# Performance work log

Hardware: AMD Instinct MI355X
Metric: run time of the kernel (lower is better)

Reference implementation:

```python
import jax, jax.numpy as jnp
import numpy as np

TOP_K = 2

def setup_inputs() -> dict:
    key = jax.random.key(0)
    k1, k2 = jax.random.split(key)
    T, D, E = 16384, 2048, 64  # num_tokens, d_model, num_experts
    x = jax.random.normal(k1, (T, D), dtype=jnp.float32)
    Wg = jax.random.normal(k2, (D, E), dtype=jnp.float32) / np.sqrt(D)
    return {"x": x, "Wg": Wg}

def reference(x, Wg):
    T, E = x.shape[0], Wg.shape[1]
    # gate logits + softmax over experts
    logits = x @ Wg                                   # [T, E]
    probs = jax.nn.softmax(logits, axis=-1)           # [T, E]
    # top-k expert selection, renormalize selected weights
    top_vals, top_idx = jax.lax.top_k(probs, TOP_K)   # [T, K]
    top_vals = top_vals / jnp.sum(top_vals, axis=-1, keepdims=True)
    # scatter sparse gate weights into dense [T, E]
    rows = jnp.arange(T)[:, None]                     # [T, 1]
    gate_weights = jnp.zeros_like(probs).at[rows, top_idx].set(top_vals)
    # load-balance aux loss: E * sum_e f_e * P_e
    mask = jnp.sum(jax.nn.one_hot(top_idx, E, dtype=probs.dtype), axis=1)  # [T, E]
    f = jnp.mean(mask, axis=0)    # fraction of tokens routed to each expert
    P = jnp.mean(probs, axis=0)   # mean router prob per expert
    aux_loss = E * jnp.sum(f * P)
    return gate_weights, top_idx, aux_loss
```

## Files before the change

kernel.cpp:

```cpp
#include <hip/hip_runtime.h>


typedef __attribute__((ext_vector_type(8))) _Float16 half8;
typedef __attribute__((ext_vector_type(4))) float f32x4;

constexpr int DD  = 2048;
constexpr int EE  = 64;
constexpr int BM  = 16;
constexpr int BK  = 128;
constexpr int NCH = DD / BK;

#define WVM(N) asm volatile("s_waitcnt vmcnt(" #N ")" ::: "memory")
#define BAR()  asm volatile("s_barrier" ::: "memory")

__global__ __launch_bounds__(256) void wsplit_kernel(
    const float* __restrict__ Wg, _Float16* __restrict__ wF)
{
    __shared__ float xl[32][65];
    const int tid = threadIdx.x;
    const int kc  = blockIdx.x;
    const int k0  = kc * 32;
#pragma unroll
    for (int r = 0; r < 2; ++r) {
        int slot = tid + r * 256;
        int row = slot >> 4, c4 = (slot & 15) << 2;
        *(float4*)&xl[row][c4] = *(const float4*)&Wg[(size_t)(k0 + row) * EE + c4];
    }
    __syncthreads();
    const int t = tid >> 6, l = tid & 63;
    const int e  = t * 16 + (l & 15);
    const int kl = (l >> 4) * 8;
    half8 hh, ll;
#pragma unroll
    for (int j = 0; j < 8; ++j) {
        float v = xl[kl + j][e];
        _Float16 h = (_Float16)v;
        hh[j] = h;
        ll[j] = (_Float16)((v - (float)h) * 4096.f);
    }
    const size_t base = (size_t)(kc * 8 + t * 2) * 512 + (size_t)l * 8;
    *(half8*)&wF[base]       = hh;
    *(half8*)&wF[base + 512] = ll;
}

__global__ __launch_bounds__(256, 4) void gate_kernel(
    const float* __restrict__ x, const _Float16* __restrict__ wF,
    float* __restrict__ gate_out, float* __restrict__ idx_out,
    float* __restrict__ pSum, float* __restrict__ pCnt)
{
    __shared__ __align__(16) union {
        float xs[3][BM][BK];
        struct { float red[4][BM][68]; float auxsm[2][4][64]; } ep;
    } sm;

    const int tid  = threadIdx.x;
    const int kq   = tid >> 6;
    const int lane = tid & 63;
    const size_t tok0 = (size_t)blockIdx.x * BM;
    const float* xg = x + tok0 * DD;

    auto stageX = [&](int buf, int c) {
#pragma unroll
        for (int r = 0; r < 2; ++r) {
            int slot = tid + r * 256;
            int row  = slot >> 5;
            int cb   = (slot & 31) << 4;
            int sb   = cb ^ ((row & 7) << 5);
            __builtin_amdgcn_global_load_lds(
                xg + (size_t)row * DD + c * BK + (sb >> 2),
                &sm.xs[buf][row][cb >> 2], 16, 0, 0);
        }
    };

    f32x4 aH[4], aL[4];
#pragma unroll
    for (int t = 0; t < 4; ++t) {
        aH[t] = (f32x4){0.f, 0.f, 0.f, 0.f};
        aL[t] = (f32x4){0.f, 0.f, 0.f, 0.f};
    }

    const int rrow = lane & 15;
    const int rb   = (kq * 128 + ((lane >> 4) * 32)) ^ ((rrow & 7) << 5);

    auto compute = [&](int buf, int c) {
        const _Float16* wb = wF + (size_t)(c * 4 + kq) * 4096 + (size_t)lane * 8;
        half8 wh[4], wl[4];
#pragma unroll
        for (int t = 0; t < 4; ++t) {
            wh[t] = *(const half8*)(wb + (t * 2) * 512);
            wl[t] = *(const half8*)(wb + (t * 2 + 1) * 512);
        }
        const float* p = (const float*)((const char*)&sm.xs[buf][rrow][0] + rb);
        float4 xa = *(const float4*)p;
        float4 xb = *(const float4*)(p + 4);
        half8 ah, al;
        {
            float v;
            v = xa.x; { _Float16 h=(_Float16)v; ah[0]=h; al[0]=(_Float16)((v-(float)h)*4096.f); }
            v = xa.y; { _Float16 h=(_Float16)v; ah[1]=h; al[1]=(_Float16)((v-(float)h)*4096.f); }
            v = xa.z; { _Float16 h=(_Float16)v; ah[2]=h; al[2]=(_Float16)((v-(float)h)*4096.f); }
            v = xa.w; { _Float16 h=(_Float16)v; ah[3]=h; al[3]=(_Float16)((v-(float)h)*4096.f); }
            v = xb.x; { _Float16 h=(_Float16)v; ah[4]=h; al[4]=(_Float16)((v-(float)h)*4096.f); }
            v = xb.y; { _Float16 h=(_Float16)v; ah[5]=h; al[5]=(_Float16)((v-(float)h)*4096.f); }
            v = xb.z; { _Float16 h=(_Float16)v; ah[6]=h; al[6]=(_Float16)((v-(float)h)*4096.f); }
            v = xb.w; { _Float16 h=(_Float16)v; ah[7]=h; al[7]=(_Float16)((v-(float)h)*4096.f); }
        }
#pragma unroll
        for (int t = 0; t < 4; ++t) {
            aH[t] = __builtin_amdgcn_mfma_f32_16x16x32_f16(ah, wh[t], aH[t], 0, 0, 0);
            aL[t] = __builtin_amdgcn_mfma_f32_16x16x32_f16(ah, wl[t], aL[t], 0, 0, 0);
            aL[t] = __builtin_amdgcn_mfma_f32_16x16x32_f16(al, wh[t], aL[t], 0, 0, 0);
        }
    };

    stageX(0, 0);
    stageX(1, 1);

#pragma unroll 1
    for (int c = 0; c < NCH; ++c) {
        if (c < NCH - 1) { WVM(2); } else { WVM(0); }
        BAR();
        compute(c % 3, c);
        if (c + 2 < NCH) stageX((c + 2) % 3, c + 2);
    }

    __syncthreads();
    const float inv = 1.f / 4096.f;
#pragma unroll
    for (int e = 0; e < 4; ++e) {
        const int row = (lane >> 4) * 4 + e;
#pragma unroll
        for (int t = 0; t < 4; ++t)
            sm.ep.red[kq][row][t * 16 + (lane & 15)] = aH[t][e] + aL[t][e] * inv;
    }
    __syncthreads();

    float sumP_acc = 0.f;
    float cnt_acc  = 0.f;
#pragma unroll 1
    for (int tt = 0; tt < 4; ++tt) {
        const int tl = kq * 4 + tt;
        const size_t t = tok0 + tl;
        float v = (sm.ep.red[0][tl][lane] + sm.ep.red[1][tl][lane])
                + (sm.ep.red[2][tl][lane] + sm.ep.red[3][tl][lane]);

        float m = v;
#pragma unroll
        for (int off = 32; off; off >>= 1) m = fmaxf(m, __shfl_xor(m, off, 64));
        float p = expf(v - m);
        float s = p;
#pragma unroll
        for (int off = 32; off; off >>= 1) s += __shfl_xor(s, off, 64);
        float prob = p / s;
        sumP_acc += prob;

        float bv = prob; int bi = lane;
#pragma unroll
        for (int off = 32; off; off >>= 1) {
            float ov = __shfl_xor(bv, off, 64);
            int   oi = __shfl_xor(bi, off, 64);
            if (ov > bv || (ov == bv && oi < bi)) { bv = ov; bi = oi; }
        }
        float v2 = (lane == bi) ? -1.f : prob;
        float bv2 = v2; int bi2 = lane;
#pragma unroll
        for (int off = 32; off; off >>= 1) {
            float ov = __shfl_xor(bv2, off, 64);
            int   oi = __shfl_xor(bi2, off, 64);
            if (ov > bv2 || (ov == bv2 && oi < bi2)) { bv2 = ov; bi2 = oi; }
        }

        float denom = bv + bv2;
        float g1 = bv / denom, g2 = bv2 / denom;
        float g = (lane == bi) ? g1 : ((lane == bi2) ? g2 : 0.f);
        gate_out[t * EE + lane] = g;
        if (lane == 0) {
            idx_out[2 * t]     = (float)bi;
            idx_out[2 * t + 1] = (float)bi2;
        }
        cnt_acc += (lane == bi)  ? 1.f : 0.f;
        cnt_acc += (lane == bi2) ? 1.f : 0.f;
    }

    sm.ep.auxsm[0][kq][lane] = sumP_acc;
    sm.ep.auxsm[1][kq][lane] = cnt_acc;
    __syncthreads();
    if (kq == 0) {
        float sp = 0.f, c2 = 0.f;
#pragma unroll
        for (int w = 0; w < 4; ++w) {
            sp += sm.ep.auxsm[0][w][lane];
            c2 += sm.ep.auxsm[1][w][lane];
        }
        pSum[(size_t)blockIdx.x * 64 + lane] = sp;
        pCnt[(size_t)blockIdx.x * 64 + lane] = c2;
    }
}

__global__ __launch_bounds__(256) void aux1_kernel(
    const float* __restrict__ pSum, const float* __restrict__ pCnt,
    float* __restrict__ p2Sum, float* __restrict__ p2Cnt)
{
    const int tid  = threadIdx.x;
    const int wv   = tid >> 6;
    const int lane = tid & 63;
    __shared__ float smem[2][4][64];

    const int r0 = blockIdx.x * 16 + wv * 4;
    float sp = 0.f, cc = 0.f;
#pragma unroll
    for (int u = 0; u < 4; ++u) {
        sp += pSum[(size_t)(r0 + u) * 64 + lane];
        cc += pCnt[(size_t)(r0 + u) * 64 + lane];
    }
    smem[0][wv][lane] = sp;
    smem[1][wv][lane] = cc;
    __syncthreads();
    if (wv == 0) {
        float SP = smem[0][0][lane] + smem[0][1][lane]
                 + smem[0][2][lane] + smem[0][3][lane];
        float CC = smem[1][0][lane] + smem[1][1][lane]
                 + smem[1][2][lane] + smem[1][3][lane];
        p2Sum[(size_t)blockIdx.x * 64 + lane] = SP;
        p2Cnt[(size_t)blockIdx.x * 64 + lane] = CC;
    }
}

__global__ __launch_bounds__(256) void aux2_kernel(
    const float* __restrict__ p2Sum, const float* __restrict__ p2Cnt,
    float* __restrict__ aux_out, float scale)
{
    const int tid  = threadIdx.x;
    const int wv   = tid >> 6;
    const int lane = tid & 63;
    __shared__ float smem[2][4][64];

    float sp = 0.f, cc = 0.f;
#pragma unroll 1
    for (int b = wv * 16; b < wv * 16 + 16; ++b) {
        sp += p2Sum[(size_t)b * 64 + lane];
        cc += p2Cnt[(size_t)b * 64 + lane];
    }
    smem[0][wv][lane] = sp;
    smem[1][wv][lane] = cc;
    __syncthreads();
    if (wv == 0) {
        float SP = smem[0][0][lane] + smem[0][1][lane]
                 + smem[0][2][lane] + smem[0][3][lane];
        float CC = smem[1][0][lane] + smem[1][1][lane]
                 + smem[1][2][lane] + smem[1][3][lane];
        float prod = SP * CC;
#pragma unroll
        for (int off = 32; off; off >>= 1) prod += __shfl_xor(prod, off, 64);
        if (lane == 0) aux_out[0] = prod * scale;
    }
}

extern "C" void kernel_launch(void* const* d_in, const int* in_sizes, int n_in,
                              void* d_out, int out_size, void* d_ws, size_t ws_size,
                              hipStream_t stream) {
    const float* x  = (const float*)d_in[0];
    const float* Wg = (const float*)d_in[1];
    const int T = in_sizes[0] / DD;

    float* out      = (float*)d_out;
    float* gate_out = out;
    float* idx_out  = out + (size_t)T * EE;
    float* aux_out  = idx_out + (size_t)T * 2;

    const int nblocks = T / BM;
    _Float16* wF = (_Float16*)d_ws;
    float* pSum  = (float*)(wF + (size_t)64 * 8 * 512);
    float* pCnt  = pSum + (size_t)nblocks * 64;
    float* p2Sum = pCnt + (size_t)nblocks * 64;
    float* p2Cnt = p2Sum + 64 * 64;

    wsplit_kernel<<<64, 256, 0, stream>>>(Wg, wF);
    gate_kernel<<<nblocks, 256, 0, stream>>>(x, wF, gate_out, idx_out, pSum, pCnt);

    const float scale = (float)EE / ((float)T * (float)T);
    aux1_kernel<<<64, 256, 0, stream>>>(pSum, pCnt, p2Sum, p2Cnt);
    aux2_kernel<<<1, 256, 0, stream>>>(p2Sum, p2Cnt, aux_out, scale);
}
```

Measured before the change: 54.85 us.

## Split gate GEMM along K across two blocks and move softmax/top-k to finish kernel

The gate GEMM is now split-K by two: each token tile is handled by two blocks that each cover half of d_model and write partial logits to workspace. A new finish kernel sums the two partials and does the softmax, top-2 selection, scatter and aux partial sums, and the two-stage aux reduction becomes a single stage. The x staging pipeline drops from triple to double buffering, and the W fragment loads are split into two halves. The aim is more blocks and parallelism for the memory-bound GEMM, at the cost of a partial-logit round trip through global memory, an extra launch and a shallower prefetch.

```diff
diff --git a/kernel.cpp b/kernel.cpp
--- a/kernel.cpp
+++ b/kernel.cpp
@@ -8,7 +8,7 @@
 constexpr int EE  = 64;
 constexpr int BM  = 16;
 constexpr int BK  = 128;
-constexpr int NCH = DD / BK;
+constexpr int NCH = 8;
 
 #define WVM(N) asm volatile("s_waitcnt vmcnt(" #N ")" ::: "memory")
 #define BAR()  asm volatile("s_barrier" ::: "memory")
@@ -45,19 +45,20 @@
 
 __global__ __launch_bounds__(256, 4) void gate_kernel(
     const float* __restrict__ x, const _Float16* __restrict__ wF,
-    float* __restrict__ gate_out, float* __restrict__ idx_out,
-    float* __restrict__ pSum, float* __restrict__ pCnt)
+    float* __restrict__ partial)
 {
     __shared__ __align__(16) union {
-        float xs[3][BM][BK];
-        struct { float red[4][BM][68]; float auxsm[2][4][64]; } ep;
+        float xs[2][BM][BK];
+        float red[4][BM][65];
     } sm;
 
     const int tid  = threadIdx.x;
     const int kq   = tid >> 6;
     const int lane = tid & 63;
-    const size_t tok0 = (size_t)blockIdx.x * BM;
-    const float* xg = x + tok0 * DD;
+    const int tile = blockIdx.x >> 1;
+    const int kb   = blockIdx.x & 1;
+    const size_t tok0 = (size_t)tile * BM;
+    const float* xg = x + tok0 * DD + kb * 1024;
 
     auto stageX = [&](int buf, int c) {
 #pragma unroll
@@ -83,13 +84,8 @@
     const int rb   = (kq * 128 + ((lane >> 4) * 32)) ^ ((rrow & 7) << 5);
 
     auto compute = [&](int buf, int c) {
-        const _Float16* wb = wF + (size_t)(c * 4 + kq) * 4096 + (size_t)lane * 8;
-        half8 wh[4], wl[4];
-#pragma unroll
-        for (int t = 0; t < 4; ++t) {
-            wh[t] = *(const half8*)(wb + (t * 2) * 512);
-            wl[t] = *(const half8*)(wb + (t * 2 + 1) * 512);
-        }
+        const _Float16* wb = wF + (size_t)(kb * 32 + c * 4 + kq) * 4096
+                                + (size_t)lane * 8;
         const float* p = (const float*)((const char*)&sm.xs[buf][rrow][0] + rb);
         float4 xa = *(const float4*)p;
         float4 xb = *(const float4*)(p + 4);
@@ -105,23 +101,39 @@
             v = xb.z; { _Float16 h=(_Float16)v; ah[6]=h; al[6]=(_Float16)((v-(float)h)*4096.f); }
             v = xb.w; { _Float16 h=(_Float16)v; ah[7]=h; al[7]=(_Float16)((v-(float)h)*4096.f); }
         }
-#pragma unroll
-        for (int t = 0; t < 4; ++t) {
-            aH[t] = __builtin_amdgcn_mfma_f32_16x16x32_f16(ah, wh[t], aH[t], 0, 0, 0);
-            aL[t] = __builtin_amdgcn_mfma_f32_16x16x32_f16(ah, wl[t], aL[t], 0, 0, 0);
-            aL[t] = __builtin_amdgcn_mfma_f32_16x16x32_f16(al, wh[t], aL[t], 0, 0, 0);
+        {
+            half8 wh0 = *(const half8*)(wb + 0 * 512);
+            half8 wl0 = *(const half8*)(wb + 1 * 512);
+            half8 wh1 = *(const half8*)(wb + 2 * 512);
+            half8 wl1 = *(const half8*)(wb + 3 * 512);
+            aH[0] = __builtin_amdgcn_mfma_f32_16x16x32_f16(ah, wh0, aH[0], 0, 0, 0);
+            aL[0] = __builtin_amdgcn_mfma_f32_16x16x32_f16(ah, wl0, aL[0], 0, 0, 0);
+            aL[0] = __builtin_amdgcn_mfma_f32_16x16x32_f16(al, wh0, aL[0], 0, 0, 0);
+            aH[1] = __builtin_amdgcn_mfma_f32_16x16x32_f16(ah, wh1, aH[1], 0, 0, 0);
+            aL[1] = __builtin_amdgcn_mfma_f32_16x16x32_f16(ah, wl1, aL[1], 0, 0, 0);
+            aL[1] = __builtin_amdgcn_mfma_f32_16x16x32_f16(al, wh1, aL[1], 0, 0, 0);
+        }
+        {
+            half8 wh2 = *(const half8*)(wb + 4 * 512);
+            half8 wl2 = *(const half8*)(wb + 5 * 512);
+            half8 wh3 = *(const half8*)(wb + 6 * 512);
+            half8 wl3 = *(const half8*)(wb + 7 * 512);
+            aH[2] = __builtin_amdgcn_mfma_f32_16x16x32_f16(ah, wh2, aH[2], 0, 0, 0);
+            aL[2] = __builtin_amdgcn_mfma_f32_16x16x32_f16(ah, wl2, aL[2], 0, 0, 0);
+            aL[2] = __builtin_amdgcn_mfma_f32_16x16x32_f16(al, wh2, aL[2], 0, 0, 0);
+            aH[3] = __builtin_amdgcn_mfma_f32_16x16x32_f16(ah, wh3, aH[3], 0, 0, 0);
+            aL[3] = __builtin_amdgcn_mfma_f32_16x16x32_f16(ah, wl3, aL[3], 0, 0, 0);
+            aL[3] = __builtin_amdgcn_mfma_f32_16x16x32_f16(al, wh3, aL[3], 0, 0, 0);
         }
     };
 
     stageX(0, 0);
-    stageX(1, 1);
-
 #pragma unroll 1
     for (int c = 0; c < NCH; ++c) {
-        if (c < NCH - 1) { WVM(2); } else { WVM(0); }
+        WVM(0);
         BAR();
-        compute(c % 3, c);
-        if (c + 2 < NCH) stageX((c + 2) % 3, c + 2);
+        if (c + 1 < NCH) stageX((c + 1) & 1, c + 1);
+        compute(c & 1, c);
     }
 
     __syncthreads();
@@ -131,18 +143,39 @@
         const int row = (lane >> 4) * 4 + e;
 #pragma unroll
         for (int t = 0; t < 4; ++t)
-            sm.ep.red[kq][row][t * 16 + (lane & 15)] = aH[t][e] + aL[t][e] * inv;
-    }
-    __syncthreads();
+            sm.red[kq][row][t * 16 + (lane & 15)] = aH[t][e] + aL[t][e] * inv;
+    }
+    __syncthreads();
+
+    float* pb = partial + (size_t)blockIdx.x * (BM * EE);
+#pragma unroll
+    for (int rr = 0; rr < 4; ++rr) {
+        const int row = kq * 4 + rr;
+        float v = (sm.red[0][row][lane] + sm.red[1][row][lane])
+                + (sm.red[2][row][lane] + sm.red[3][row][lane]);
+        pb[row * EE + lane] = v;
+    }
+}
+
+__global__ __launch_bounds__(256) void finish_kernel(
+    const float* __restrict__ partial,
+    float* __restrict__ gate_out, float* __restrict__ idx_out,
+    float* __restrict__ pSum, float* __restrict__ pCnt)
+{
+    const int tid  = threadIdx.x;
+    const int wv   = tid >> 6;
+    const int lane = tid & 63;
+    __shared__ float auxsm[2][4][64];
 
     float sumP_acc = 0.f;
     float cnt_acc  = 0.f;
 #pragma unroll 1
-    for (int tt = 0; tt < 4; ++tt) {
-        const int tl = kq * 4 + tt;
-        const size_t t = tok0 + tl;
-        float v = (sm.ep.red[0][tl][lane] + sm.ep.red[1][tl][lane])
-                + (sm.ep.red[2][tl][lane] + sm.ep.red[3][tl][lane]);
+    for (int tt = 0; tt < 16; ++tt) {
+        const size_t t    = (size_t)blockIdx.x * 64 + wv * 16 + tt;
+        const size_t tile = t >> 4;
+        const int    row  = (int)(t & 15);
+        const float* pb = partial + tile * 2 * (BM * EE) + row * EE;
+        float v = pb[lane] + pb[BM * EE + lane];
 
         float m = v;
 #pragma unroll
@@ -182,64 +215,33 @@
         cnt_acc += (lane == bi2) ? 1.f : 0.f;
     }
 
-    sm.ep.auxsm[0][kq][lane] = sumP_acc;
-    sm.ep.auxsm[1][kq][lane] = cnt_acc;
-    __syncthreads();
-    if (kq == 0) {
-        float sp = 0.f, c2 = 0.f;
-#pragma unroll
-        for (int w = 0; w < 4; ++w) {
-            sp += sm.ep.auxsm[0][w][lane];
-            c2 += sm.ep.auxsm[1][w][lane];
-        }
+    auxsm[0][wv][lane] = sumP_acc;
+    auxsm[1][wv][lane] = cnt_acc;
+    __syncthreads();
+    if (wv == 0) {
+        float sp = auxsm[0][0][lane] + auxsm[0][1][lane]
+                 + auxsm[0][2][lane] + auxsm[0][3][lane];
+        float cc = auxsm[1][0][lane] + auxsm[1][1][lane]
+                 + auxsm[1][2][lane] + auxsm[1][3][lane];
         pSum[(size_t)blockIdx.x * 64 + lane] = sp;
-        pCnt[(size_t)blockIdx.x * 64 + lane] = c2;
-    }
-}
-
-__global__ __launch_bounds__(256) void aux1_kernel(
+        pCnt[(size_t)blockIdx.x * 64 + lane] = cc;
+    }
+}
+
+__global__ __launch_bounds__(256) void aux2_kernel(
     const float* __restrict__ pSum, const float* __restrict__ pCnt,
-    float* __restrict__ p2Sum, float* __restrict__ p2Cnt)
+    float* __restrict__ aux_out, float scale)
 {
     const int tid  = threadIdx.x;
     const int wv   = tid >> 6;
     const int lane = tid & 63;
     __shared__ float smem[2][4][64];
 
-    const int r0 = blockIdx.x * 16 + wv * 4;
-    float sp = 0.f, cc = 0.f;
-#pragma unroll
-    for (int u = 0; u < 4; ++u) {
-        sp += pSum[(size_t)(r0 + u) * 64 + lane];
-        cc += pCnt[(size_t)(r0 + u) * 64 + lane];
-    }
-    smem[0][wv][lane] = sp;
-    smem[1][wv][lane] = cc;
-    __syncthreads();
-    if (wv == 0) {
-        float SP = smem[0][0][lane] + smem[0][1][lane]
-                 + smem[0][2][lane] + smem[0][3][lane];
-        float CC = smem[1][0][lane] + smem[1][1][lane]
-                 + smem[1][2][lane] + smem[1][3][lane];
-        p2Sum[(size_t)blockIdx.x * 64 + lane] = SP;
-        p2Cnt[(size_t)blockIdx.x * 64 + lane] = CC;
-    }
-}
-
-__global__ __launch_bounds__(256) void aux2_kernel(
-    const float* __restrict__ p2Sum, const float* __restrict__ p2Cnt,
-    float* __restrict__ aux_out, float scale)
-{
-    const int tid  = threadIdx.x;
-    const int wv   = tid >> 6;
-    const int lane = tid & 63;
-    __shared__ float smem[2][4][64];
-
     float sp = 0.f, cc = 0.f;
 #pragma unroll 1
-    for (int b = wv * 16; b < wv * 16 + 16; ++b) {
-        sp += p2Sum[(size_t)b * 64 + lane];
-        cc += p2Cnt[(size_t)b * 64 + lane];
+    for (int b = wv; b < 256; b += 4) {
+        sp += pSum[(size_t)b * 64 + lane];
+        cc += pCnt[(size_t)b * 64 + lane];
     }
     smem[0][wv][lane] = sp;
     smem[1][wv][lane] = cc;
@@ -268,17 +270,16 @@
     float* idx_out  = out + (size_t)T * EE;
     float* aux_out  = idx_out + (size_t)T * 2;
 
-    const int nblocks = T / BM;
-    _Float16* wF = (_Float16*)d_ws;
-    float* pSum  = (float*)(wF + (size_t)64 * 8 * 512);
-    float* pCnt  = pSum + (size_t)nblocks * 64;
-    float* p2Sum = pCnt + (size_t)nblocks * 64;
-    float* p2Cnt = p2Sum + 64 * 64;
+    const int ntiles = T / BM;
+    _Float16* wF   = (_Float16*)d_ws;
+    float* partial = (float*)(wF + (size_t)64 * 8 * 512);
+    float* pSum    = partial + (size_t)ntiles * 2 * BM * EE;
+    float* pCnt    = pSum + 256 * 64;
 
     wsplit_kernel<<<64, 256, 0, stream>>>(Wg, wF);
-    gate_kernel<<<nblocks, 256, 0, stream>>>(x, wF, gate_out, idx_out, pSum, pCnt);
-
+    gate_kernel<<<ntiles * 2, 256, 0, stream>>>(x, wF, partial);
+    finish_kernel<<<T / 64, 256, 0, stream>>>(partial, gate_out, idx_out,
+                                              pSum, pCnt);
     const float scale = (float)EE / ((float)T * (float)T);
-    aux1_kernel<<<64, 256, 0, stream>>>(pSum, pCnt, p2Sum, p2Cnt);
-    aux2_kernel<<<1, 256, 0, stream>>>(p2Sum, p2Cnt, aux_out, scale);
-}
+    aux2_kernel<<<1, 256, 0, stream>>>(pSum, pCnt, aux_out, scale);
+}
```

After: 90.64 us. +65.2%, slower.
